# Performance work log

Hardware: AMD Instinct MI355X
Metric: run time of the kernel (lower is better)

The kernel has to match this reference:

```python
import jax, jax.numpy as jnp
import numpy as np

W_LEFT, W_RIGHT = 3, 0
HEADS = 16
L, D_IN, D_OUT = 16384, 2048, 2048


def setup_inputs() -> dict:
    key = jax.random.key(0)
    k0, k1, k2, k3, k4 = jax.random.split(key, 5)
    d_head = D_OUT // HEADS
    e_seq = jax.random.normal(k0, (L, D_IN), jnp.float32)
    q_param = jax.random.normal(k1, (HEADS, d_head), jnp.float32)
    # Linear weights stored as (in, out); bias only on the output projection.
    Wk = jax.random.normal(k2, (D_IN, D_OUT), jnp.float32) * (1.0 / np.sqrt(D_IN))
    Wv = jax.random.normal(k3, (D_IN, D_OUT), jnp.float32) * (1.0 / np.sqrt(D_IN))
    Wo = jax.random.normal(k4, (D_OUT, D_OUT), jnp.float32) * (1.0 / np.sqrt(D_OUT))
    bo = jnp.zeros((D_OUT,), jnp.float32)
    return {"e_seq": e_seq, "q_param": q_param, "Wk": Wk, "Wv": Wv, "Wo": Wo, "bo": bo}


def reference(e_seq, q_param, Wk, Wv, Wo, bo):
    Lx, _ = e_seq.shape
    H, d_head = q_param.shape
    D_out = H * d_head
    k_all = (e_seq @ Wk).reshape(Lx, H, d_head)  # [L,H,d]
    v_all = (e_seq @ Wv).reshape(Lx, H, d_head)
    scale = 1.0 / np.sqrt(d_head).astype(np.float32)

    # Vectorized sliding window: for each t, window indices t-W_LEFT .. t+W_RIGHT
    offs = jnp.arange(-W_LEFT, W_RIGHT + 1)              # [W]
    idx = jnp.arange(Lx)[:, None] + offs[None, :]        # [L,W]
    valid = (idx >= 0) & (idx < Lx)                      # boundary mask
    idxc = jnp.clip(idx, 0, Lx - 1)
    k_win = k_all[idxc]                                  # [L,W,H,d]
    v_win = v_all[idxc]                                  # [L,W,H,d]

    att = jnp.einsum('hd,lwhd->lhw', q_param, k_win) * scale  # [L,H,W]
    att = jnp.where(valid[:, None, :], att, -jnp.inf)
    w = jax.nn.softmax(att, axis=-1)
    pooled = jnp.einsum('lhw,lwhd->lhd', w, v_win).reshape(Lx, D_out)
    return pooled @ Wo + bo
```

## Files before the change

### kernel.cpp

```cpp
#include <hip/hip_runtime.h>
#include <hip/hip_bf16.h>

#define L_SEQ   16384
#define D_IO    2048
#define HEADS   16
#define DHEAD   128
#define KDIM    2048
#define KT64    (KDIM / 64)

typedef __attribute__((ext_vector_type(8))) short short8;
typedef __attribute__((ext_vector_type(4))) float floatx4;

typedef const __attribute__((address_space(1))) unsigned int gu_t;
typedef __attribute__((address_space(3))) unsigned int lu_t;

__device__ __forceinline__ unsigned short f2bf(float f) {
  unsigned u = __float_as_uint(f);
  u += 0x7fffu + ((u >> 16) & 1u);
  return (unsigned short)(u >> 16);
}
__device__ __forceinline__ float bf2f(unsigned short s) {
  return __uint_as_float(((unsigned)s) << 16);
}

__global__ __launch_bounds__(256)
void prep(const float* __restrict__ e_seq,
          const float* __restrict__ q,
          const float* __restrict__ Wk,
          const float* __restrict__ Wv,
          const float* __restrict__ Wo,
          unsigned short* __restrict__ Ebf,
          unsigned short* __restrict__ Wvt,
          unsigned short* __restrict__ Wot,
          unsigned short* __restrict__ QKbf)
{
  __shared__ float tile[32][33];
  const int b = blockIdx.x;
  if (b < 8192) {
    const long n = (long)L_SEQ * D_IO;
    for (long i = ((long)b * 256 + threadIdx.x) * 8; i < n; i += (long)8192 * 256 * 8) {
      const float4 v0 = *(const float4*)(e_seq + i);
      const float4 v1 = *(const float4*)(e_seq + i + 4);
      uint4 r;
      r.x = (unsigned)f2bf(v0.x) | ((unsigned)f2bf(v0.y) << 16);
      r.y = (unsigned)f2bf(v0.z) | ((unsigned)f2bf(v0.w) << 16);
      r.z = (unsigned)f2bf(v1.x) | ((unsigned)f2bf(v1.y) << 16);
      r.w = (unsigned)f2bf(v1.z) | ((unsigned)f2bf(v1.w) << 16);
      *(uint4*)(Ebf + i) = r;
    }
  } else if (b < 16384) {
    const int tb  = b - 8192;
    const int mat = tb >> 12;
    const int idx = tb & 4095;
    const float* S = (mat == 0) ? Wv : Wo;
    unsigned short* D = (mat == 0) ? Wvt : Wot;
    const int bn = (idx & 63) * 32;
    const int bk = (idx >> 6) * 32;
    const int tx = threadIdx.x & 31, ty = threadIdx.x >> 5;
    #pragma unroll
    for (int i = 0; i < 32; i += 8)
      tile[ty + i][tx] = S[(size_t)(bk + ty + i) * D_IO + bn + tx];
    __syncthreads();
    #pragma unroll
    for (int i = 0; i < 32; i += 8)
      D[(size_t)(bn + ty + i) * D_IO + bk + tx] = f2bf(tile[tx][ty + i]);
  } else {
    const int tb = b - 16384;
    const int h = tb >> 3, chunk = tb & 7;
    const int i = chunk * 256 + threadIdx.x;
    const float* wrow = Wk + (size_t)i * D_IO + h * DHEAD;
    const float* qrow = q + h * DHEAD;
    float s = 0.f;
    #pragma unroll
    for (int d = 0; d < DHEAD; d += 4) {
      const float4 wv4 = *(const float4*)(wrow + d);
      const float4 qv4 = *(const float4*)(qrow + d);
      s += wv4.x * qv4.x + wv4.y * qv4.y + wv4.z * qv4.z + wv4.w * qv4.w;
    }
    QKbf[h * D_IO + i] = f2bf(s);
  }
}

__global__ __launch_bounds__(256)
void scores(const unsigned short* __restrict__ Ebf,
            const unsigned short* __restrict__ QK,
            float* __restrict__ S)
{
  const int lane = threadIdx.x & 63, wave = threadIdx.x >> 6;
  const int row0 = (blockIdx.x * 4 + wave) * 16;
  const int fr = lane & 15, ko = (lane >> 4) * 8;
  const unsigned short* ea = Ebf + (size_t)(row0 + fr) * KDIM + ko;
  const unsigned short* qa = QK + (size_t)fr * KDIM + ko;
  floatx4 acc = (floatx4)0.f;
  #pragma unroll 8
  for (int kt = 0; kt < KDIM / 32; ++kt) {
    const short8 av = *(const short8*)(ea + kt * 32);
    const short8 bv = *(const short8*)(qa + kt * 32);
    acc = __builtin_amdgcn_mfma_f32_16x16x32_bf16(av, bv, acc, 0, 0, 0);
  }
  #pragma unroll
  for (int r = 0; r < 4; ++r)
    S[(size_t)(row0 + (lane >> 4) * 4 + r) * HEADS + fr] = acc[r];
}

template<int EPI>
__global__ __launch_bounds__(512, 2)
void gemm256(const unsigned short* __restrict__ A,
             const unsigned short* __restrict__ B,
             void* __restrict__ Cout,
             const float* __restrict__ bias,
             const int ldc, const int bnShift)
{
  __shared__ unsigned short lds[65536];

  const int t = threadIdx.x, lane = t & 63, wave = t >> 6;
  const int wm = wave >> 2, wn = wave & 3;

  const int nwg  = (int)(gridDim.x * gridDim.y);
  const int flat = (int)(blockIdx.y * gridDim.x + blockIdx.x);
  const int cpx  = nwg >> 3;
  const int swz  = (flat & 7) * cpx + (flat >> 3);
  const int bn = swz & ((1 << bnShift) - 1);
  const int bm = swz >> bnShift;

  const int fr = lane & 15, kq = lane >> 4;
  const int sl0 = ((kq ^ (fr & 7)) & 7) * 8;

  const int srow  = t >> 3;
  const int sslot = (((t & 7) ^ (srow & 7)) & 7) * 8;
  const unsigned short* aSrc = A + (size_t)(bm * 256 + srow) * KDIM + sslot;
  const unsigned short* bSrc = B + (size_t)(bn * 256 + srow) * KDIM + sslot;

  floatx4 acc[8][4];
  #pragma unroll
  for (int m = 0; m < 8; ++m)
    #pragma unroll
    for (int n = 0; n < 4; ++n) acc[m][n] = (floatx4)0.f;

#define STAGE1(srcbase, q, dstoff, ts)                                                        \
    __builtin_amdgcn_global_load_lds((gu_t*)((srcbase) + (size_t)(ts) * 64 +                  \
                                             (size_t)(q) * 64 * KDIM),                        \
                                     (lu_t*)(lds + (dstoff) + wave * 512), 16, 0, 0)

  STAGE1(aSrc, 0, 0, 0);      STAGE1(aSrc, 2, 8192, 0);
  STAGE1(bSrc, 0, 16384, 0);  STAGE1(bSrc, 1, 20480, 0);
  STAGE1(bSrc, 2, 24576, 0);  STAGE1(bSrc, 3, 28672, 0);
  STAGE1(aSrc, 1, 4096, 0);   STAGE1(aSrc, 3, 12288, 0);
  asm volatile("s_waitcnt vmcnt(2)" ::: "memory");
  __builtin_amdgcn_s_barrier();

  short8 aq[4][2], bq0[2][2], bq1[2][2];

  for (int tt = 0; tt < KT64; ++tt) {
    const int s = tt & 1;
    const int ts = (tt + 1 < KT64) ? (tt + 1) : tt;
    const int d = (s ^ 1) * 32768;
    const unsigned short* As = lds + s * 32768;
    const unsigned short* Bs = As + 16384;
    const unsigned short* ArLo = As + (wm * 2) * 4096 + fr * 64;
    const unsigned short* ArHi = ArLo + 4096;
    const unsigned short* Br   = Bs + wn * 4096 + fr * 64;

    #pragma unroll
    for (int m = 0; m < 4; ++m) {
      aq[m][0] = *(const short8*)(ArLo + m * 1024 + sl0);
      aq[m][1] = *(const short8*)(ArLo + m * 1024 + (sl0 ^ 32));
    }
    #pragma unroll
    for (int n = 0; n < 2; ++n) {
      bq0[n][0] = *(const short8*)(Br + n * 1024 + sl0);
      bq0[n][1] = *(const short8*)(Br + n * 1024 + (sl0 ^ 32));
    }
    STAGE1(aSrc, 0, d, ts);
    STAGE1(aSrc, 2, d + 8192, ts);
    __builtin_amdgcn_s_barrier();
    asm volatile("s_waitcnt lgkmcnt(0)" ::: "memory");
    __builtin_amdgcn_sched_barrier(0);
    __builtin_amdgcn_s_setprio(1);
    #pragma unroll
    for (int m = 0; m < 4; ++m)
      #pragma unroll
      for (int n = 0; n < 2; ++n) {
        acc[m][n] = __builtin_amdgcn_mfma_f32_16x16x32_bf16(aq[m][0], bq0[n][0], acc[m][n], 0, 0, 0);
        acc[m][n] = __builtin_amdgcn_mfma_f32_16x16x32_bf16(aq[m][1], bq0[n][1], acc[m][n], 0, 0, 0);
      }
    __builtin_amdgcn_s_setprio(0);
    __builtin_amdgcn_s_barrier();

    #pragma unroll
    for (int n = 0; n < 2; ++n) {
      bq1[n][0] = *(const short8*)(Br + (2 + n) * 1024 + sl0);
      bq1[n][1] = *(const short8*)(Br + (2 + n) * 1024 + (sl0 ^ 32));
    }
    STAGE1(bSrc, 0, d + 16384, ts);
    STAGE1(bSrc, 1, d + 20480, ts);
    __builtin_amdgcn_s_barrier();
    asm volatile("s_waitcnt lgkmcnt(0)" ::: "memory");
    __builtin_amdgcn_sched_barrier(0);
    __builtin_amdgcn_s_setprio(1);
    #pragma unroll
    for (int m = 0; m < 4; ++m)
      #pragma unroll
      for (int n = 0; n < 2; ++n) {
        acc[m][2 + n] = __builtin_amdgcn_mfma_f32_16x16x32_bf16(aq[m][0], bq1[n][0], acc[m][2 + n], 0, 0, 0);
        acc[m][2 + n] = __builtin_amdgcn_mfma_f32_16x16x32_bf16(aq[m][1], bq1[n][1], acc[m][2 + n], 0, 0, 0);
      }
    __builtin_amdgcn_s_setprio(0);
    asm volatile("s_waitcnt vmcnt(4)" ::: "memory");
    __builtin_amdgcn_s_barrier();

    #pragma unroll
    for (int m = 0; m < 4; ++m) {
      aq[m][0] = *(const short8*)(ArHi + m * 1024 + sl0);
      aq[m][1] = *(const short8*)(ArHi + m * 1024 + (sl0 ^ 32));
    }
    STAGE1(bSrc, 2, d + 24576, ts);
    STAGE1(bSrc, 3, d + 28672, ts);
    __builtin_amdgcn_s_barrier();
    asm volatile("s_waitcnt lgkmcnt(0)" ::: "memory");
    __builtin_amdgcn_sched_barrier(0);
    __builtin_amdgcn_s_setprio(1);
    #pragma unroll
    for (int m = 0; m < 4; ++m)
      #pragma unroll
      for (int n = 0; n < 2; ++n) {
        acc[4 + m][2 + n] = __builtin_amdgcn_mfma_f32_16x16x32_bf16(aq[m][0], bq1[n][0], acc[4 + m][2 + n], 0, 0, 0);
        acc[4 + m][2 + n] = __builtin_amdgcn_mfma_f32_16x16x32_bf16(aq[m][1], bq1[n][1], acc[4 + m][2 + n], 0, 0, 0);
      }
    __builtin_amdgcn_s_setprio(0);
    __builtin_amdgcn_s_barrier();

    STAGE1(aSrc, 1, d + 4096, ts);
    STAGE1(aSrc, 3, d + 12288, ts);
    __builtin_amdgcn_s_setprio(1);
    #pragma unroll
    for (int m = 0; m < 4; ++m)
      #pragma unroll
      for (int n = 0; n < 2; ++n) {
        acc[4 + m][n] = __builtin_amdgcn_mfma_f32_16x16x32_bf16(aq[m][0], bq0[n][0], acc[4 + m][n], 0, 0, 0);
        acc[4 + m][n] = __builtin_amdgcn_mfma_f32_16x16x32_bf16(aq[m][1], bq0[n][1], acc[4 + m][n], 0, 0, 0);
      }
    __builtin_amdgcn_s_setprio(0);
    asm volatile("s_waitcnt vmcnt(2)" ::: "memory");
    __builtin_amdgcn_s_barrier();
  }
#undef STAGE1

  asm volatile("s_waitcnt vmcnt(0)" ::: "memory");

  const int crow0 = bm * 256 + wm * 128 + kq * 4;
  const int ccol0 = bn * 256 + wn * 64 + fr;
  if (EPI == 0) {
    unsigned short* C = (unsigned short*)Cout;
    #pragma unroll
    for (int m = 0; m < 8; ++m)
      #pragma unroll
      for (int n = 0; n < 4; ++n)
        #pragma unroll
        for (int r = 0; r < 4; ++r)
          C[(size_t)(crow0 + m * 16 + r) * ldc + ccol0 + n * 16] = f2bf(acc[m][n][r]);
  } else {
    float* C = (float*)Cout;
    #pragma unroll
    for (int n = 0; n < 4; ++n) {
      const float bv_ = bias[ccol0 + n * 16];
      #pragma unroll
      for (int m = 0; m < 8; ++m)
        #pragma unroll
        for (int r = 0; r < 4; ++r)
          C[(size_t)(crow0 + m * 16 + r) * ldc + ccol0 + n * 16] = acc[m][n][r] + bv_;
    }
  }
}

__global__ __launch_bounds__(256)
void winpool(const unsigned short* __restrict__ V,
             const float* __restrict__ S,
             unsigned short* __restrict__ P)
{
  const int lane = threadIdx.x & 63, wid = threadIdx.x >> 6;
  const int bx = ((int)blockIdx.x & 7) * ((int)gridDim.x >> 3) + ((int)blockIdx.x >> 3);
  const int t = bx * 4 + wid;
  const int h = blockIdx.y;
  const float scale = 0.08838834764831845f;

  float s[4];
  #pragma unroll
  for (int w = 0; w < 4; ++w) {
    const int idx = t - 3 + w;
    s[w] = (idx >= 0) ? S[(size_t)idx * HEADS + h] * scale : -3.0e38f;
  }
  float mx = fmaxf(fmaxf(s[0], s[1]), fmaxf(s[2], s[3]));
  float p[4], sum = 0.f;
  #pragma unroll
  for (int w = 0; w < 4; ++w) {
    p[w] = (t - 3 + w >= 0) ? expf(s[w] - mx) : 0.f;
    sum += p[w];
  }
  const float inv = 1.f / sum;

  float o0 = 0.f, o1 = 0.f;
  #pragma unroll
  for (int w = 0; w < 4; ++w) {
    const int idx = t - 3 + w;
    if (idx >= 0) {
      const unsigned vv = *(const unsigned*)(V + (size_t)idx * D_IO + h * DHEAD + lane * 2);
      o0 += p[w] * bf2f((unsigned short)(vv & 0xffffu));
      o1 += p[w] * bf2f((unsigned short)(vv >> 16));
    }
  }
  o0 *= inv; o1 *= inv;
  const unsigned outw = ((unsigned)f2bf(o1) << 16) | (unsigned)f2bf(o0);
  *(unsigned*)(P + (size_t)t * D_IO + h * DHEAD + lane * 2) = outw;
}

extern "C" void kernel_launch(void* const* d_in, const int* in_sizes, int n_in,
                              void* d_out, int out_size, void* d_ws, size_t ws_size,
                              hipStream_t stream)
{
  const float* e_seq = (const float*)d_in[0];
  const float* q     = (const float*)d_in[1];
  const float* Wk    = (const float*)d_in[2];
  const float* Wv    = (const float*)d_in[3];
  const float* Wo    = (const float*)d_in[4];
  const float* bo    = (const float*)d_in[5];
  float* out = (float*)d_out;

  char* ws = (char*)d_ws;
  unsigned short* Ebf  = (unsigned short*)ws;
  unsigned short* Vbf  = (unsigned short*)(ws + 67108864);
  unsigned short* Wvt  = (unsigned short*)(ws + 134217728);
  unsigned short* Wot  = (unsigned short*)(ws + 142606336);
  unsigned short* QKbf = (unsigned short*)(ws + 150994944);
  float*          Sbuf = (float*)(ws + 151060480);

  prep<<<16512, 256, 0, stream>>>(e_seq, q, Wk, Wv, Wo, Ebf, Wvt, Wot, QKbf);

  gemm256<0><<<dim3(8, 64), 512, 0, stream>>>(Ebf, Wvt, Vbf, nullptr, 2048, 3);

  scores<<<L_SEQ / 64, 256, 0, stream>>>(Ebf, QKbf, Sbuf);

  winpool<<<dim3(L_SEQ / 4, HEADS), 256, 0, stream>>>(Vbf, Sbuf, Ebf);

  gemm256<1><<<dim3(8, 64), 512, 0, stream>>>(Ebf, Wot, out, bo, 2048, 3);
}
```

Before: 415.3 us.

## Fuse scores GEMV into V-projection GEMM epilogue and batch winpool rows per wave

Removes the separate scores kernel launch and computes the per-head scores inside the V-projection GEMM, in the tail of blocks with bn==0, reading A rows directly from global memory. Winpool now processes 8 consecutive timesteps per wave, reusing overlapping window loads of S and V and using fast __expf. This saves a launch and cuts redundant V/S reads, but it adds tail work to one column of GEMM blocks, which may create load imbalance, and it drops the block-index swizzle in winpool.

New measurement: 418.3 us. Within noise of the previous version (+0.7%).

```diff
diff --git a/kernel.cpp b/kernel.cpp
--- a/kernel.cpp
+++ b/kernel.cpp
@@ -81,35 +81,15 @@
   }
 }
 
-__global__ __launch_bounds__(256)
-void scores(const unsigned short* __restrict__ Ebf,
-            const unsigned short* __restrict__ QK,
-            float* __restrict__ S)
-{
-  const int lane = threadIdx.x & 63, wave = threadIdx.x >> 6;
-  const int row0 = (blockIdx.x * 4 + wave) * 16;
-  const int fr = lane & 15, ko = (lane >> 4) * 8;
-  const unsigned short* ea = Ebf + (size_t)(row0 + fr) * KDIM + ko;
-  const unsigned short* qa = QK + (size_t)fr * KDIM + ko;
-  floatx4 acc = (floatx4)0.f;
-  #pragma unroll 8
-  for (int kt = 0; kt < KDIM / 32; ++kt) {
-    const short8 av = *(const short8*)(ea + kt * 32);
-    const short8 bv = *(const short8*)(qa + kt * 32);
-    acc = __builtin_amdgcn_mfma_f32_16x16x32_bf16(av, bv, acc, 0, 0, 0);
-  }
-  #pragma unroll
-  for (int r = 0; r < 4; ++r)
-    S[(size_t)(row0 + (lane >> 4) * 4 + r) * HEADS + fr] = acc[r];
-}
-
-template<int EPI>
+template<int EPI, int SCORES>
 __global__ __launch_bounds__(512, 2)
 void gemm256(const unsigned short* __restrict__ A,
              const unsigned short* __restrict__ B,
              void* __restrict__ Cout,
              const float* __restrict__ bias,
-             const int ldc, const int bnShift)
+             const int ldc, const int bnShift,
+             const unsigned short* __restrict__ QK,
+             float* __restrict__ Sout)
 {
   __shared__ unsigned short lds[65536];
 
@@ -271,6 +251,25 @@
           C[(size_t)(crow0 + m * 16 + r) * ldc + ccol0 + n * 16] = acc[m][n][r] + bv_;
     }
   }
+
+  if (SCORES && bn == 0) {
+    const int r0 = bm * 256 + wave * 32;
+    const unsigned short* ea0 = A + (size_t)(r0 + fr) * KDIM + kq * 8;
+    const unsigned short* ea1 = ea0 + (size_t)16 * KDIM;
+    const unsigned short* qa  = QK + (size_t)fr * KDIM + kq * 8;
+    floatx4 s0 = (floatx4)0.f, s1 = (floatx4)0.f;
+    #pragma unroll 4
+    for (int kt = 0; kt < KDIM / 32; ++kt) {
+      const short8 bvq = *(const short8*)(qa + kt * 32);
+      s0 = __builtin_amdgcn_mfma_f32_16x16x32_bf16(*(const short8*)(ea0 + kt * 32), bvq, s0, 0, 0, 0);
+      s1 = __builtin_amdgcn_mfma_f32_16x16x32_bf16(*(const short8*)(ea1 + kt * 32), bvq, s1, 0, 0, 0);
+    }
+    #pragma unroll
+    for (int r = 0; r < 4; ++r) {
+      Sout[(size_t)(r0 + kq * 4 + r) * HEADS + fr]      = s0[r];
+      Sout[(size_t)(r0 + 16 + kq * 4 + r) * HEADS + fr] = s1[r];
+    }
+  }
 }
 
 __global__ __launch_bounds__(256)
@@ -279,39 +278,36 @@
              unsigned short* __restrict__ P)
 {
   const int lane = threadIdx.x & 63, wid = threadIdx.x >> 6;
-  const int bx = ((int)blockIdx.x & 7) * ((int)gridDim.x >> 3) + ((int)blockIdx.x >> 3);
-  const int t = bx * 4 + wid;
+  const int tg = (int)blockIdx.x * 4 + wid;
+  const int t0 = tg * 8;
   const int h = blockIdx.y;
   const float scale = 0.08838834764831845f;
 
-  float s[4];
+  float sv[11], v0[11], v1[11];
   #pragma unroll
-  for (int w = 0; w < 4; ++w) {
-    const int idx = t - 3 + w;
-    s[w] = (idx >= 0) ? S[(size_t)idx * HEADS + h] * scale : -3.0e38f;
-  }
-  float mx = fmaxf(fmaxf(s[0], s[1]), fmaxf(s[2], s[3]));
-  float p[4], sum = 0.f;
+  for (int i = 0; i < 11; ++i) {
+    const int idx = t0 - 3 + i;
+    if (idx >= 0) {
+      sv[i] = S[(size_t)idx * HEADS + h] * scale;
+      const unsigned vv = *(const unsigned*)(V + (size_t)idx * D_IO + h * DHEAD + lane * 2);
+      v0[i] = bf2f((unsigned short)(vv & 0xffffu));
+      v1[i] = bf2f((unsigned short)(vv >> 16));
+    } else {
+      sv[i] = -3.0e38f; v0[i] = 0.f; v1[i] = 0.f;
+    }
+  }
+
   #pragma unroll
-  for (int w = 0; w < 4; ++w) {
-    p[w] = (t - 3 + w >= 0) ? expf(s[w] - mx) : 0.f;
-    sum += p[w];
-  }
-  const float inv = 1.f / sum;
-
-  float o0 = 0.f, o1 = 0.f;
-  #pragma unroll
-  for (int w = 0; w < 4; ++w) {
-    const int idx = t - 3 + w;
-    if (idx >= 0) {
-      const unsigned vv = *(const unsigned*)(V + (size_t)idx * D_IO + h * DHEAD + lane * 2);
-      o0 += p[w] * bf2f((unsigned short)(vv & 0xffffu));
-      o1 += p[w] * bf2f((unsigned short)(vv >> 16));
-    }
-  }
-  o0 *= inv; o1 *= inv;
-  const unsigned outw = ((unsigned)f2bf(o1) << 16) | (unsigned)f2bf(o0);
-  *(unsigned*)(P + (size_t)t * D_IO + h * DHEAD + lane * 2) = outw;
+  for (int j = 0; j < 8; ++j) {
+    const float mx = fmaxf(fmaxf(sv[j], sv[j + 1]), fmaxf(sv[j + 2], sv[j + 3]));
+    float p0 = __expf(sv[j] - mx),     p1 = __expf(sv[j + 1] - mx);
+    float p2 = __expf(sv[j + 2] - mx), p3 = __expf(sv[j + 3] - mx);
+    const float inv = 1.f / (p0 + p1 + p2 + p3);
+    const float o0 = (p0 * v0[j] + p1 * v0[j + 1] + p2 * v0[j + 2] + p3 * v0[j + 3]) * inv;
+    const float o1 = (p0 * v1[j] + p1 * v1[j + 1] + p2 * v1[j + 2] + p3 * v1[j + 3]) * inv;
+    const unsigned outw = ((unsigned)f2bf(o1) << 16) | (unsigned)f2bf(o0);
+    *(unsigned*)(P + (size_t)(t0 + j) * D_IO + h * DHEAD + lane * 2) = outw;
+  }
 }
 
 extern "C" void kernel_launch(void* const* d_in, const int* in_sizes, int n_in,
@@ -336,11 +332,9 @@
 
   prep<<<16512, 256, 0, stream>>>(e_seq, q, Wk, Wv, Wo, Ebf, Wvt, Wot, QKbf);
 
-  gemm256<0><<<dim3(8, 64), 512, 0, stream>>>(Ebf, Wvt, Vbf, nullptr, 2048, 3);
-
-  scores<<<L_SEQ / 64, 256, 0, stream>>>(Ebf, QKbf, Sbuf);
-
-  winpool<<<dim3(L_SEQ / 4, HEADS), 256, 0, stream>>>(Vbf, Sbuf, Ebf);
-
-  gemm256<1><<<dim3(8, 64), 512, 0, stream>>>(Ebf, Wot, out, bo, 2048, 3);
-}
+  gemm256<0, 1><<<dim3(8, 64), 512, 0, stream>>>(Ebf, Wvt, Vbf, nullptr, 2048, 3, QKbf, Sbuf);
+
+  winpool<<<dim3(512, HEADS), 256, 0, stream>>>(Vbf, Sbuf, Ebf);
+
+  gemm256<1, 0><<<dim3(8, 64), 512, 0, stream>>>(Ebf, Wot, out, bo, 2048, 3, nullptr, nullptr);
+}
```
